# Kernel optimization log

Hardware: AMD Instinct MI355X
Metric: run time of the kernel (lower is better)

## Reference

```python
import jax, jax.numpy as jnp
import numpy as np

D_MODEL = 1024
D_STATE = 16
D_CONV = 4
EXPAND = 2
D_INNER = D_MODEL * EXPAND
B = 1
L = 2048


def setup_inputs() -> dict:
    key = jax.random.key(0)
    ks = jax.random.split(key, 8)
    s = lambda k, shape, scale: jax.random.normal(k, shape, dtype=jnp.float32) * scale
    return {
        "x": jax.random.normal(ks[0], (B, L, D_MODEL), dtype=jnp.float32),
        "in_proj_w": s(ks[1], (D_INNER * 2, D_MODEL), D_MODEL ** -0.5),
        "conv_w": s(ks[2], (D_INNER, 1, D_CONV), D_CONV ** -0.5),  # depthwise [O, I/g=1, K]
        "conv_b": jnp.zeros((D_INNER,), jnp.float32),
        "x_proj_w": s(ks[3], (2 * D_STATE + 1, D_INNER), D_INNER ** -0.5),
        "dt_proj_w": s(ks[4], (D_INNER, 1), 1.0),
        "dt_proj_b": jnp.zeros((D_INNER,), jnp.float32),
        "A_log": jnp.log(jnp.broadcast_to(jnp.arange(1, D_STATE + 1, dtype=jnp.float32), (D_INNER, D_STATE))),
        "D": jnp.ones((D_INNER,), jnp.float32),
        "out_proj_w": s(ks[5], (D_MODEL, D_INNER), D_INNER ** -0.5),
    }


def reference(x, in_proj_w, conv_w, conv_b, x_proj_w, dt_proj_w, dt_proj_b, A_log, D, out_proj_w):
    Bb = x.shape[0]
    # in_proj -> split into ssm branch and gate z
    xz = x @ in_proj_w.T                      # [B, L, 2*Di]
    x_ssm, z = jnp.split(xz, 2, axis=-1)
    # causal depthwise conv1d (torch pads K-1 both sides then slices [:L] == left-pad K-1)
    xt = jnp.swapaxes(x_ssm, 1, 2)            # [B, Di, L]
    xc = jax.lax.conv_general_dilated(
        xt, conv_w, window_strides=(1,), padding=[(D_CONV - 1, 0)],
        feature_group_count=D_INNER, dimension_numbers=("NCH", "OIH", "NCH"))
    xc = xc + conv_b[None, :, None]
    xc = jax.nn.silu(jnp.swapaxes(xc, 1, 2))  # [B, L, Di]
    # selective SSM
    A = -jnp.exp(A_log)                        # [Di, N]
    xp = xc @ x_proj_w.T                       # [B, L, 1+2N]
    dt_r = xp[..., :1]
    Bv = xp[..., 1:1 + D_STATE]                # [B, L, N]
    Cv = xp[..., 1 + D_STATE:]                 # [B, L, N]
    dt = jax.nn.softplus(dt_r @ dt_proj_w.T + dt_proj_b)   # [B, L, Di]
    dA = jnp.exp(dt[..., None] * A)                          # [B, L, Di, N]
    dBx = dt[..., None] * Bv[:, :, None, :] * xc[..., None]  # [B, L, Di, N]

    def step(h, inps):
        dA_t, dBx_t, C_t = inps
        h = dA_t * h + dBx_t                   # [B, Di, N]
        y = jnp.einsum("bdn,bn->bd", h, C_t)
        return h, y

    h0 = jnp.zeros((Bb, D_INNER, D_STATE), x.dtype)
    _, ys = jax.lax.scan(step, h0, (jnp.swapaxes(dA, 0, 1), jnp.swapaxes(dBx, 0, 1), jnp.swapaxes(Cv, 0, 1)))
    y = jnp.swapaxes(ys, 0, 1) + xc * D        # [B, L, Di]
    return (y * jax.nn.silu(z)) @ out_proj_w.T
```

## Files before the change

kernel.cpp:

```cpp
#include <hip/hip_runtime.h>
#include <math.h>

#define L_SEQ   2048
#define DM      1024
#define DI      2048
#define NST     16
#define LC      32
#define NCHUNK  64
#define XP_LD   36
#define KSPLIT  8
#define LOG2E   1.44269504f

typedef short s16x8 __attribute__((ext_vector_type(8)));
typedef unsigned short u16x8 __attribute__((ext_vector_type(8)));
typedef float f32x4 __attribute__((ext_vector_type(4)));

__device__ __forceinline__ float silu_f(float x) {
  return x / (1.0f + __expf(-x));
}
__device__ __forceinline__ float softplus_f(float x) {
  return x > 20.0f ? x : __logf(1.0f + __expf(x));
}
__device__ __forceinline__ ushort f2bf(float f) {
  unsigned int u = __float_as_uint(f);
  unsigned int r = (u + 0x7fffu + ((u >> 16) & 1u)) >> 16;
  return (ushort)r;
}
__device__ __forceinline__ float bf2f(ushort u) {
  return __uint_as_float((unsigned int)u << 16);
}
__device__ __forceinline__ void gload_lds16(const void* g, void* lds) {
  __builtin_amdgcn_global_load_lds(
      (const __attribute__((address_space(1))) unsigned int*)g,
      (__attribute__((address_space(3))) unsigned int*)lds,
      16, 0, 0);
}

__global__ __launch_bounds__(256) void cvt_bf16_k(
    const float* __restrict__ in, ushort* __restrict__ out, int n4) {
  int i = blockIdx.x * 256 + threadIdx.x;
  if (i >= n4) return;
  float4 v = ((const float4*)in)[i];
  ushort4 o;
  o.x = f2bf(v.x); o.y = f2bf(v.y); o.z = f2bf(v.z); o.w = f2bf(v.w);
  ((ushort4*)out)[i] = o;
}

template <int MFRAG, bool BF16OUT>
__global__ __launch_bounds__(256) void gemm_mfma_bf16(
    const ushort* __restrict__ A, const ushort* __restrict__ B,
    void* __restrict__ Cv, int K, int ldc) {
  constexpr int BM = MFRAG * 32;
  __shared__ ushort As[BM * 32];
  __shared__ ushort Bs[128 * 32];
  const int tid  = threadIdx.x;
  const int lane = tid & 63;
  const int wv   = tid >> 6;
  const int wr   = wv >> 1;
  const int wc   = wv & 1;
  const int m0 = blockIdx.y * BM;
  const int n0 = blockIdx.x * 128;

  f32x4 acc[MFRAG][4] = {};
  const int kc = (tid & 3) * 8;

  for (int k0 = 0; k0 < K; k0 += 32) {
    __syncthreads();
#pragma unroll
    for (int q = 0; q < BM / 64; ++q) {
      int id = q * 256 + tid;
      int m  = id >> 2;
      gload_lds16(A + (size_t)(m0 + m) * K + k0 + kc, (char*)As + id * 16);
    }
#pragma unroll
    for (int q = 0; q < 2; ++q) {
      int id = q * 256 + tid;
      int n  = id >> 2;
      gload_lds16(B + (size_t)(n0 + n) * K + k0 + kc, (char*)Bs + id * 16);
    }
    __syncthreads();

    s16x8 af[MFRAG], bfr[4];
#pragma unroll
    for (int m = 0; m < MFRAG; ++m)
      af[m] = *(const s16x8*)&As[(wr * MFRAG * 16 + m * 16 + (lane & 15)) * 32 + (lane >> 4) * 8];
#pragma unroll
    for (int n = 0; n < 4; ++n)
      bfr[n] = *(const s16x8*)&Bs[(wc * 64 + n * 16 + (lane & 15)) * 32 + (lane >> 4) * 8];
#pragma unroll
    for (int m = 0; m < MFRAG; ++m)
#pragma unroll
      for (int n = 0; n < 4; ++n)
        acc[m][n] = __builtin_amdgcn_mfma_f32_16x16x32_bf16(af[m], bfr[n], acc[m][n], 0, 0, 0);
  }
  const int cr = (lane >> 4) * 4;
  const int cc = lane & 15;
#pragma unroll
  for (int m = 0; m < MFRAG; ++m) {
    int gr0 = m0 + wr * MFRAG * 16 + m * 16 + cr;
#pragma unroll
    for (int n = 0; n < 4; ++n) {
      int gc = n0 + wc * 64 + n * 16 + cc;
#pragma unroll
      for (int r = 0; r < 4; ++r) {
        if constexpr (BF16OUT)
          ((ushort*)Cv)[(size_t)(gr0 + r) * ldc + gc] = f2bf(acc[m][n][r]);
        else
          ((float*)Cv)[(size_t)(gr0 + r) * ldc + gc] = acc[m][n][r];
      }
    }
  }
}

__global__ __launch_bounds__(256) void conv_silu_T_k(
    const ushort* __restrict__ xzb, const float* __restrict__ cw,
    const float* __restrict__ cb, float* __restrict__ xcT) {
  const int d0  = blockIdx.x * 64;
  const int l0  = blockIdx.y * 64;
  const int tid = threadIdx.x;
  __shared__ ushort xt[67][64];
  __shared__ float  ot[64][65];
#pragma unroll
  for (int q = 0; q < 3; ++q) {
    int id = q * 256 + tid;
    if (id < 67 * 8) {
      int row = id >> 3, c8 = (id & 7) * 8;
      int l = l0 - 3 + row;
      u16x8 v = (u16x8)(ushort)0;
      if (l >= 0)
        v = *(const u16x8*)&xzb[(size_t)l * 4096 + d0 + c8];
      *(u16x8*)&xt[row][c8] = v;
    }
  }
  __syncthreads();
  const int dloc = tid & 63;
  const int d    = d0 + dloc;
  const float w0 = cw[d*4+0], w1 = cw[d*4+1], w2 = cw[d*4+2], w3 = cw[d*4+3];
  const float bb = cb[d];
  const int lb = (tid >> 6) * 16;
#pragma unroll
  for (int j = 0; j < 16; ++j) {
    int ll = lb + j;
    float a = bb;
    a = fmaf(w0, bf2f(xt[ll+0][dloc]), a);
    a = fmaf(w1, bf2f(xt[ll+1][dloc]), a);
    a = fmaf(w2, bf2f(xt[ll+2][dloc]), a);
    a = fmaf(w3, bf2f(xt[ll+3][dloc]), a);
    ot[dloc][ll] = silu_f(a);
  }
  __syncthreads();
#pragma unroll
  for (int q = 0; q < 4; ++q) {
    int f4 = q * 256 + tid;
    int dr = f4 >> 4, lc = (f4 & 15) * 4;
    float4 v = make_float4(ot[dr][lc], ot[dr][lc+1], ot[dr][lc+2], ot[dr][lc+3]);
    *(float4*)&xcT[(size_t)(d0 + dr) * L_SEQ + l0 + lc] = v;
  }
}

__global__ __launch_bounds__(256) void gemm_xp_k(
    const float* __restrict__ xcT, const float* __restrict__ Wxp,
    float* __restrict__ xp_part) {
  const int L0   = blockIdx.x * 64;
  const int ks   = blockIdx.y;
  const int wv   = threadIdx.x >> 6;
  const int lane = threadIdx.x & 63;
  __shared__ float xcs[64][65];
  __shared__ float Ws[36][64];
  float acc[9] = {};
  const int kbeg = ks * (DI / KSPLIT);
  const int kend = kbeg + DI / KSPLIT;
  for (int k0 = kbeg; k0 < kend; k0 += 64) {
#pragma unroll
    for (int q = 0; q < 4; ++q) {
      int f4 = q * 256 + threadIdx.x;
      int dr = f4 >> 4;
      int lc = (f4 & 15) * 4;
      float4 v = *(const float4*)&xcT[(size_t)(k0 + dr) * L_SEQ + L0 + lc];
      xcs[lc+0][dr] = v.x; xcs[lc+1][dr] = v.y;
      xcs[lc+2][dr] = v.z; xcs[lc+3][dr] = v.w;
    }
    for (int idx = threadIdx.x; idx < 36 * 16; idx += 256) {
      int j = idx >> 4; int cc = (idx & 15) << 2;
      float4 v = make_float4(0.f, 0.f, 0.f, 0.f);
      if (j < 33) v = *(const float4*)&Wxp[(size_t)j * DI + k0 + cc];
      *(float4*)&Ws[j][cc] = v;
    }
    __syncthreads();
#pragma unroll 4
    for (int kk = 0; kk < 64; kk += 4) {
      float4 wr[9];
#pragma unroll
      for (int jj = 0; jj < 9; ++jj) wr[jj] = *(const float4*)&Ws[wv*9 + jj][kk];
      float a0 = xcs[lane][kk+0], a1 = xcs[lane][kk+1];
      float a2 = xcs[lane][kk+2], a3 = xcs[lane][kk+3];
#pragma unroll
      for (int jj = 0; jj < 9; ++jj) {
        acc[jj] = fmaf(a0, wr[jj].x, acc[jj]);
        acc[jj] = fmaf(a1, wr[jj].y, acc[jj]);
        acc[jj] = fmaf(a2, wr[jj].z, acc[jj]);
        acc[jj] = fmaf(a3, wr[jj].w, acc[jj]);
      }
    }
    __syncthreads();
  }
  const int l = L0 + lane;
#pragma unroll
  for (int jj = 0; jj < 9; ++jj) {
    int j = wv * 9 + jj;
    if (j < 33)
      xp_part[(size_t)ks * L_SEQ * XP_LD + (size_t)l * XP_LD + j] = acc[jj];
  }
}

__global__ __launch_bounds__(256) void reduce_xp_k(
    const float* __restrict__ part, float* __restrict__ xp) {
  int i = blockIdx.x * 256 + threadIdx.x;
  float s = 0.f;
#pragma unroll
  for (int ks = 0; ks < KSPLIT; ++ks)
    s += part[(size_t)ks * L_SEQ * XP_LD + i];
  xp[i] = s;
}

__device__ __forceinline__ void stage_xps(
    float (*xps)[36], const float* __restrict__ xp, int l0, int tid) {
  for (int idx = tid; idx < LC * 33; idx += 256) {
    int rr = idx / 33, j = idx - rr * 33;
    int col = (j == 0) ? 32 : j - 1;
    xps[rr][col] = xp[(size_t)(l0 + rr) * XP_LD + j];
  }
}
__device__ __forceinline__ void stage_xcs64(
    float (*xcs)[LC + 1], const float* __restrict__ xcT, int d0, int l0, int tid) {
#pragma unroll
  for (int q = 0; q < 2; ++q) {
    int f4  = q * 256 + tid;
    int row = f4 >> 3;
    int col = (f4 & 7) * 4;
    float4 v = *(const float4*)&xcT[(size_t)(d0 + row) * L_SEQ + l0 + col];
    xcs[row][col+0] = v.x; xcs[row][col+1] = v.y;
    xcs[row][col+2] = v.z; xcs[row][col+3] = v.w;
  }
}
__device__ __forceinline__ void stage_dts64(
    float (*dts)[64], const float* __restrict__ xp,
    const float* __restrict__ dtw, const float* __restrict__ dtb,
    int d0, int l0, int tid) {
  int dd = tid & 63;
  int tb = (tid >> 6) * 8;
  float wv = dtw[d0 + dd], bv = dtb[d0 + dd];
#pragma unroll
  for (int j = 0; j < 8; ++j)
    dts[tb + j][dd] = softplus_f(fmaf(xp[(size_t)(l0 + tb + j) * XP_LD], wv, bv));
}

__global__ __launch_bounds__(256, 4) void scan_partial_k(
    const float* __restrict__ xcT, const float* __restrict__ xp,
    const float* __restrict__ dtw, const float* __restrict__ dtb,
    const float* __restrict__ A_log,
    float* __restrict__ P, float* __restrict__ Q) {
  const int tid = threadIdx.x;
  const int dl  = tid >> 2;
  const int nq  = (tid & 3) * 4;
  const int d0  = blockIdx.x * 64;
  const int d   = d0 + dl;
  const int c   = blockIdx.y;
  const int l0  = c * LC;
  __shared__ float xps[LC][36];
  __shared__ float xcs[64][LC + 1];
  __shared__ float dts[LC][64];
  stage_xps(xps, xp, l0, tid);
  stage_xcs64(xcs, xcT, d0, l0, tid);
  stage_dts64(dts, xp, dtw, dtb, d0, l0, tid);

  float4 Av = *(const float4*)&A_log[(size_t)d * NST + nq];
  float Ad2[4] = { -__expf(Av.x) * LOG2E, -__expf(Av.y) * LOG2E,
                   -__expf(Av.z) * LOG2E, -__expf(Av.w) * LOG2E };
  float h[4] = {0.f, 0.f, 0.f, 0.f};
  float sumdt = 0.f;
  __syncthreads();
#pragma unroll 4
  for (int t = 0; t < LC; ++t) {
    float dt  = dts[t][dl];
    sumdt += dt;
    float dtx = dt * xcs[dl][t];
    f32x4 B = *(const f32x4*)&xps[t][nq];
#pragma unroll
    for (int n = 0; n < 4; ++n) {
      float da = exp2f(dt * Ad2[n]);
      h[n] = fmaf(da, h[n], dtx * B[n]);
    }
  }
  size_t base = ((size_t)c * DI + d) * NST + nq;
  *(float4*)&P[base] = make_float4(exp2f(sumdt * Ad2[0]), exp2f(sumdt * Ad2[1]),
                                   exp2f(sumdt * Ad2[2]), exp2f(sumdt * Ad2[3]));
  *(float4*)&Q[base] = make_float4(h[0], h[1], h[2], h[3]);
}

__global__ __launch_bounds__(256) void scan_prefix_k(
    const float* __restrict__ P, float* __restrict__ QHs) {
  const int g = blockIdx.x * 256 + threadIdx.x;
  const int d = g >> 2;
  const int q = (g & 3) << 2;
  float4 h = make_float4(0.f, 0.f, 0.f, 0.f);
#pragma unroll 8
  for (int c = 0; c < NCHUNK; ++c) {
    size_t base = ((size_t)c * DI + d) * NST + q;
    float4 pv = *(const float4*)&P[base];
    float4 qv = *(const float4*)&QHs[base];
    *(float4*)&QHs[base] = h;
    h.x = fmaf(pv.x, h.x, qv.x);
    h.y = fmaf(pv.y, h.y, qv.y);
    h.z = fmaf(pv.z, h.z, qv.z);
    h.w = fmaf(pv.w, h.w, qv.w);
  }
}

__global__ __launch_bounds__(256, 4) void scan_final_k(
    const float* __restrict__ xcT, const float* __restrict__ xp,
    const float* __restrict__ dtw, const float* __restrict__ dtb,
    const float* __restrict__ A_log, const float* __restrict__ Dp,
    const float* __restrict__ Hs, const ushort* __restrict__ xzb,
    ushort* __restrict__ ys) {
  const int tid = threadIdx.x;
  const int dl  = tid >> 2;
  const int nq  = (tid & 3) * 4;
  const int d0  = blockIdx.x * 64;
  const int d   = d0 + dl;
  const int c   = blockIdx.y;
  const int l0  = c * LC;
  __shared__ float  xps[LC][36];
  __shared__ float  xcs[64][LC + 1];
  __shared__ float  dts[LC][64];
  __shared__ ushort zs[LC][64];
  {
    int id = tid;
    int t  = id >> 3;
    int c8 = (id & 7) * 8;
    gload_lds16(xzb + (size_t)(l0 + t) * 4096 + 2048 + d0 + c8,
                (char*)zs + id * 16);
  }
  stage_xps(xps, xp, l0, tid);
  stage_xcs64(xcs, xcT, d0, l0, tid);
  stage_dts64(dts, xp, dtw, dtb, d0, l0, tid);

  float4 Av = *(const float4*)&A_log[(size_t)d * NST + nq];
  float Ad2[4] = { -__expf(Av.x) * LOG2E, -__expf(Av.y) * LOG2E,
                   -__expf(Av.z) * LOG2E, -__expf(Av.w) * LOG2E };
  const float Dd = Dp[d];
  float h[4];
  size_t hb = ((size_t)c * DI + d) * NST + nq;
  *(float4*)&h[0] = *(const float4*)&Hs[hb];
  __syncthreads();
#pragma unroll 4
  for (int t = 0; t < LC; ++t) {
    const int l = l0 + t;
    float dt  = dts[t][dl];
    float xcv = xcs[dl][t];
    float dtx = dt * xcv;
    f32x4 B = *(const f32x4*)&xps[t][nq];
    f32x4 C = *(const f32x4*)&xps[t][16 + nq];
    float y = 0.f;
#pragma unroll
    for (int n = 0; n < 4; ++n) {
      float da = exp2f(dt * Ad2[n]);
      h[n] = fmaf(da, h[n], dtx * B[n]);
      y = fmaf(h[n], C[n], y);
    }
    y += __shfl_xor(y, 1);
    y += __shfl_xor(y, 2);
    if ((tid & 3) == 0) {
      y = fmaf(xcv, Dd, y);
      ys[(size_t)l * DI + d] = f2bf(y * silu_f(bf2f(zs[t][dl])));
    }
  }
}

extern "C" void kernel_launch(void* const* d_in, const int* in_sizes, int n_in,
                              void* d_out, int out_size, void* d_ws, size_t ws_size,
                              hipStream_t stream) {
  const float* x    = (const float*)d_in[0];
  const float* W1   = (const float*)d_in[1];
  const float* cw   = (const float*)d_in[2];
  const float* cb   = (const float*)d_in[3];
  const float* Wxp  = (const float*)d_in[4];
  const float* dtw  = (const float*)d_in[5];
  const float* dtb  = (const float*)d_in[6];
  const float* Alog = (const float*)d_in[7];
  const float* Dp   = (const float*)d_in[8];
  const float* Wout = (const float*)d_in[9];
  float* out = (float*)d_out;

  char* w = (char*)d_ws;
  ushort* xz_bf   = (ushort*)w;
  float*  xcT     = (float*)(w + 16777216);
  ushort* x_bf    = (ushort*)(w + 33554432);
  ushort* W1_bf   = (ushort*)(w + 37748736);
  float*  P       = (float*)(w + 33554432);
  float*  QHs     = (float*)(w + 41943040);
  float*  xp      = (float*)(w + 50331648);
  ushort* Wout_bf = (ushort*)(w + 50626560);
  ushort* ys_bf   = (ushort*)(w + 54820864);
  float*  xp_part = (float*)(w + 54820864);

  cvt_bf16_k<<<2048, 256, 0, stream>>>(x,    x_bf,    2048*1024/4);
  cvt_bf16_k<<<4096, 256, 0, stream>>>(W1,   W1_bf,   4096*1024/4);
  cvt_bf16_k<<<2048, 256, 0, stream>>>(Wout, Wout_bf, 1024*2048/4);
  gemm_mfma_bf16<4, true><<<dim3(4096/128, 2048/128), 256, 0, stream>>>(
      x_bf, W1_bf, xz_bf, DM, 4096);
  conv_silu_T_k<<<dim3(DI/64, L_SEQ/64), 256, 0, stream>>>(xz_bf, cw, cb, xcT);
  gemm_xp_k<<<dim3(L_SEQ/64, KSPLIT), 256, 0, stream>>>(xcT, Wxp, xp_part);
  reduce_xp_k<<<L_SEQ*XP_LD/256, 256, 0, stream>>>(xp_part, xp);
  scan_partial_k<<<dim3(DI/64, NCHUNK), 256, 0, stream>>>(xcT, xp, dtw, dtb, Alog, P, QHs);
  scan_prefix_k<<<DI*NST/4/256, 256, 0, stream>>>(P, QHs);
  scan_final_k<<<dim3(DI/64, NCHUNK), 256, 0, stream>>>(xcT, xp, dtw, dtb, Alog, Dp, QHs, xz_bf, ys_bf);
  gemm_mfma_bf16<2, false><<<dim3(1024/128, 2048/64), 256, 0, stream>>>(
      ys_bf, Wout_bf, out, DI, 1024);
}
```

Baseline: 263.3 us.

## Merge bf16 conversions, double GEMM K-tile, widen scan prefix parallelism

Fuses the three fp32-to-bf16 conversion launches into one kernel that picks its source and destination by index range. Doubles the MFMA GEMM K-tile from 32 to 64, halving the barrier and load-issue count per K, at the cost of twice the LDS. The scan prefix kernel now uses one thread per (d, n) state element instead of one per four, giving four times as many threads for the sequential chunk loop but issuing scalar instead of float4 loads and stores.

```diff
diff --git a/kernel.cpp b/kernel.cpp
--- a/kernel.cpp
+++ b/kernel.cpp
@@ -36,14 +36,20 @@
       16, 0, 0);
 }
 
-__global__ __launch_bounds__(256) void cvt_bf16_k(
-    const float* __restrict__ in, ushort* __restrict__ out, int n4) {
+__global__ __launch_bounds__(256) void cvt3_k(
+    const float* __restrict__ x, const float* __restrict__ W1,
+    const float* __restrict__ Wout,
+    ushort* __restrict__ x_bf, ushort* __restrict__ W1_bf,
+    ushort* __restrict__ Wout_bf) {
   int i = blockIdx.x * 256 + threadIdx.x;
-  if (i >= n4) return;
-  float4 v = ((const float4*)in)[i];
+  const float* src; ushort* dst; int off;
+  if (i < 524288)        { src = x;    dst = x_bf;    off = i; }
+  else if (i < 1572864)  { src = W1;   dst = W1_bf;   off = i - 524288; }
+  else                   { src = Wout; dst = Wout_bf; off = i - 1572864; }
+  float4 v = ((const float4*)src)[off];
   ushort4 o;
   o.x = f2bf(v.x); o.y = f2bf(v.y); o.z = f2bf(v.z); o.w = f2bf(v.w);
-  ((ushort4*)out)[i] = o;
+  ((ushort4*)dst)[off] = o;
 }
 
 template <int MFRAG, bool BF16OUT>
@@ -51,8 +57,8 @@
     const ushort* __restrict__ A, const ushort* __restrict__ B,
     void* __restrict__ Cv, int K, int ldc) {
   constexpr int BM = MFRAG * 32;
-  __shared__ ushort As[BM * 32];
-  __shared__ ushort Bs[128 * 32];
+  __shared__ ushort As[BM * 64];
+  __shared__ ushort Bs[128 * 64];
   const int tid  = threadIdx.x;
   const int lane = tid & 63;
   const int wv   = tid >> 6;
@@ -62,36 +68,42 @@
   const int n0 = blockIdx.x * 128;
 
   f32x4 acc[MFRAG][4] = {};
-  const int kc = (tid & 3) * 8;
-
-  for (int k0 = 0; k0 < K; k0 += 32) {
+
+  for (int k0 = 0; k0 < K; k0 += 64) {
     __syncthreads();
 #pragma unroll
-    for (int q = 0; q < BM / 64; ++q) {
-      int id = q * 256 + tid;
-      int m  = id >> 2;
-      gload_lds16(A + (size_t)(m0 + m) * K + k0 + kc, (char*)As + id * 16);
-    }
-#pragma unroll
-    for (int q = 0; q < 2; ++q) {
-      int id = q * 256 + tid;
-      int n  = id >> 2;
-      gload_lds16(B + (size_t)(n0 + n) * K + k0 + kc, (char*)Bs + id * 16);
+    for (int q = 0; q < BM / 32; ++q) {
+      int id  = q * 256 + tid;
+      int row = id >> 3;
+      gload_lds16(A + (size_t)(m0 + row) * K + k0 + (id & 7) * 8,
+                  (char*)As + id * 16);
+    }
+#pragma unroll
+    for (int q = 0; q < 4; ++q) {
+      int id  = q * 256 + tid;
+      int row = id >> 3;
+      gload_lds16(B + (size_t)(n0 + row) * K + k0 + (id & 7) * 8,
+                  (char*)Bs + id * 16);
     }
     __syncthreads();
 
-    s16x8 af[MFRAG], bfr[4];
-#pragma unroll
-    for (int m = 0; m < MFRAG; ++m)
-      af[m] = *(const s16x8*)&As[(wr * MFRAG * 16 + m * 16 + (lane & 15)) * 32 + (lane >> 4) * 8];
-#pragma unroll
-    for (int n = 0; n < 4; ++n)
-      bfr[n] = *(const s16x8*)&Bs[(wc * 64 + n * 16 + (lane & 15)) * 32 + (lane >> 4) * 8];
-#pragma unroll
-    for (int m = 0; m < MFRAG; ++m)
+#pragma unroll
+    for (int s = 0; s < 2; ++s) {
+      s16x8 af[MFRAG], bfr[4];
+#pragma unroll
+      for (int m = 0; m < MFRAG; ++m)
+        af[m] = *(const s16x8*)&As[(wr * MFRAG * 16 + m * 16 + (lane & 15)) * 64
+                                    + s * 32 + (lane >> 4) * 8];
 #pragma unroll
       for (int n = 0; n < 4; ++n)
-        acc[m][n] = __builtin_amdgcn_mfma_f32_16x16x32_bf16(af[m], bfr[n], acc[m][n], 0, 0, 0);
+        bfr[n] = *(const s16x8*)&Bs[(wc * 64 + n * 16 + (lane & 15)) * 64
+                                     + s * 32 + (lane >> 4) * 8];
+#pragma unroll
+      for (int m = 0; m < MFRAG; ++m)
+#pragma unroll
+        for (int n = 0; n < 4; ++n)
+          acc[m][n] = __builtin_amdgcn_mfma_f32_16x16x32_bf16(af[m], bfr[n], acc[m][n], 0, 0, 0);
+    }
   }
   const int cr = (lane >> 4) * 4;
   const int cc = lane & 15;
@@ -301,19 +313,16 @@
 __global__ __launch_bounds__(256) void scan_prefix_k(
     const float* __restrict__ P, float* __restrict__ QHs) {
   const int g = blockIdx.x * 256 + threadIdx.x;
-  const int d = g >> 2;
-  const int q = (g & 3) << 2;
-  float4 h = make_float4(0.f, 0.f, 0.f, 0.f);
+  const int d = g >> 4;
+  const int n = g & 15;
+  float h = 0.f;
 #pragma unroll 8
   for (int c = 0; c < NCHUNK; ++c) {
-    size_t base = ((size_t)c * DI + d) * NST + q;
-    float4 pv = *(const float4*)&P[base];
-    float4 qv = *(const float4*)&QHs[base];
-    *(float4*)&QHs[base] = h;
-    h.x = fmaf(pv.x, h.x, qv.x);
-    h.y = fmaf(pv.y, h.y, qv.y);
-    h.z = fmaf(pv.z, h.z, qv.z);
-    h.w = fmaf(pv.w, h.w, qv.w);
+    size_t base = ((size_t)c * DI + d) * NST + n;
+    float pv = P[base];
+    float qv = QHs[base];
+    QHs[base] = h;
+    h = fmaf(pv, h, qv);
   }
 }
 
@@ -404,16 +413,14 @@
   ushort* ys_bf   = (ushort*)(w + 54820864);
   float*  xp_part = (float*)(w + 54820864);
 
-  cvt_bf16_k<<<2048, 256, 0, stream>>>(x,    x_bf,    2048*1024/4);
-  cvt_bf16_k<<<4096, 256, 0, stream>>>(W1,   W1_bf,   4096*1024/4);
-  cvt_bf16_k<<<2048, 256, 0, stream>>>(Wout, Wout_bf, 1024*2048/4);
+  cvt3_k<<<8192, 256, 0, stream>>>(x, W1, Wout, x_bf, W1_bf, Wout_bf);
   gemm_mfma_bf16<4, true><<<dim3(4096/128, 2048/128), 256, 0, stream>>>(
       x_bf, W1_bf, xz_bf, DM, 4096);
   conv_silu_T_k<<<dim3(DI/64, L_SEQ/64), 256, 0, stream>>>(xz_bf, cw, cb, xcT);
   gemm_xp_k<<<dim3(L_SEQ/64, KSPLIT), 256, 0, stream>>>(xcT, Wxp, xp_part);
   reduce_xp_k<<<L_SEQ*XP_LD/256, 256, 0, stream>>>(xp_part, xp);
   scan_partial_k<<<dim3(DI/64, NCHUNK), 256, 0, stream>>>(xcT, xp, dtw, dtb, Alog, P, QHs);
-  scan_prefix_k<<<DI*NST/4/256, 256, 0, stream>>>(P, QHs);
+  scan_prefix_k<<<DI*NST/256, 256, 0, stream>>>(P, QHs);
   scan_final_k<<<dim3(DI/64, NCHUNK), 256, 0, stream>>>(xcT, xp, dtw, dtb, Alog, Dp, QHs, xz_bf, ys_bf);
   gemm_mfma_bf16<2, false><<<dim3(1024/128, 2048/64), 256, 0, stream>>>(
       ys_bf, Wout_bf, out, DI, 1024);
```

Measured after the change: 257.6 us. -2.2%, faster.
